# Kernel tuning notes

Hardware: AMD Instinct MI355X
Metric: run time of the kernel (lower is better)

Reference implementation:

```python
import jax, jax.numpy as jnp
import numpy as np

VEC_DIM = 64
RANK = 2


def setup_inputs() -> dict:
    key = jax.random.key(0)
    kg, km, kp = jax.random.split(key, 3)
    grid = jax.random.normal(kg, (193, 193, VEC_DIM), dtype=jnp.float32)
    # nn.init.uniform_(M.weight, -0.5, 0.5)
    M_weight = jax.random.uniform(km, (VEC_DIM, VEC_DIM), minval=-0.5, maxval=0.5, dtype=jnp.float32)
    # nn.init.uniform_(P, -0.1, 0.1)
    P = jax.random.uniform(kp, (VEC_DIM, VEC_DIM), minval=-0.1, maxval=0.1, dtype=jnp.float32)
    return {"grid": grid, "M_weight": M_weight, "P": P}


def reference(grid, M_weight, P):
    H, W, m = grid.shape
    # periods1[i,j] = periods2[i,j] = i*m + j + 2
    periods = (jnp.arange(m, dtype=jnp.float32)[:, None] * m
               + jnp.arange(m, dtype=jnp.float32)[None, :] + 2.0)  # [m, m]

    # ---- window extraction: linear mode (step=1), rank_mode='drop', rank_op='avg' ----
    nH = H - RANK + 1
    nW = W - RANK + 1
    win_sum = jax.lax.reduce_window(grid, 0.0, jax.lax.add,
                                    (RANK, RANK, 1), (1, 1, 1), 'VALID')  # [nH, nW, m]
    x_win = (win_sum / float(RANK * RANK)).reshape(nH * nW, m)  # [B, m]

    # ---- map through M (nn.Linear, no bias): y = x @ W^T ----
    x = x_win @ M_weight.T  # [B, m]

    # ---- phi_table gather: phi[k1,k2] = cos(2*pi*k1/periods) * cos(2*pi*k2/periods) ----
    two_pi = jnp.float32(2.0 * np.pi)
    k1s = jnp.arange(nH, dtype=jnp.float32)
    k2s = jnp.arange(nW, dtype=jnp.float32)
    cos1 = jnp.cos(two_pi * k1s[:, None, None] / periods)  # [nH, m, m]
    cos2 = jnp.cos(two_pi * k2s[:, None, None] / periods)  # [nW, m, m]
    phi = (cos1[:, None, :, :] * cos2[None, :, :, :]).reshape(nH * nW, m, m)  # [B, m, m]

    # ---- Nk = einsum('bj,ij,bij->bi', x, P, phi) ----
    Nk = jnp.einsum('bj,ij,bij->bi', x, P, phi)  # [B, m]
    return Nk
```

## Files before the change

### kernel.cpp

```cpp
#include <hip/hip_runtime.h>
#include <math.h>

#define NW 192
#define Wt 193
#define NMAIN 768
#define CHUNK 48

__device__ __forceinline__ float cos_revr(float num, float rcpden) {
    float rev = num * rcpden;
    rev = __builtin_amdgcn_fractf(rev);
    return __builtin_amdgcn_cosf(rev);
}

__global__ __launch_bounds__(256, 3) void k_fused(const float* __restrict__ grid,
                                                  const float* __restrict__ Mw,
                                                  const float* __restrict__ P,
                                                  float* __restrict__ out) {
    __shared__ float bufA[4096];
    __shared__ float bufB[4096];
    __shared__ float xls[CHUNK * 68];

    int bx = blockIdx.x;
    int k1  = bx >> 2;
    int k2s = (bx & 3) * CHUNK;
    int t = threadIdx.x;
    int lane = t & 63;
    int w = __builtin_amdgcn_readfirstlane(t >> 6);
    int jb = w * 16;

    #pragma unroll
    for (int r = 0; r < 4; ++r) {
        int e = r * 256 + t;
        ((float4*)bufB)[e] = ((const float4*)Mw)[e];
    }
    {
        int c = t & 63;
        const float* gb  = grid + ((size_t)k1 * Wt + k2s) * 64 + c;
        const float* gb1 = gb + (size_t)Wt * 64;
        #pragma unroll
        for (int r = 0; r < 12; ++r) {
            int p = w * 12 + r;
            float s = gb[p * 64] + gb[(p + 1) * 64]
                    + gb1[p * 64] + gb1[(p + 1) * 64];
            bufA[p * 68 + c] = 0.25f * s;
        }
    }
    __syncthreads();

    if (lane < 48) {
        int p = lane;
        float4 wv[16];
        #pragma unroll
        for (int q = 0; q < 16; ++q) wv[q] = *(const float4*)&bufA[p * 68 + 4 * q];
        #pragma unroll
        for (int r = 0; r < 16; ++r) {
            int j = jb + r;
            const float4* mrow = (const float4*)&bufB[j * 64];
            float acc = 0.f;
            #pragma unroll
            for (int q = 0; q < 16; ++q) {
                float4 mv = mrow[q];
                acc += wv[q].x * mv.x + wv[q].y * mv.y
                     + wv[q].z * mv.z + wv[q].w * mv.w;
            }
            xls[p * 68 + j] = acc;
        }
    }
    __syncthreads();

    {
        const float4* P4 = (const float4*)P;
        #pragma unroll
        for (int s = 0; s < 4; ++s) {
            int e = s * 256 + t;
            float4 v = P4[e];
            int i = e >> 4, j0 = (e & 15) * 4;
            bufA[(j0 + 0) * 64 + i] = v.x;
            bufA[(j0 + 1) * 64 + i] = v.y;
            bufA[(j0 + 2) * 64 + i] = v.z;
            bufA[(j0 + 3) * 64 + i] = v.w;
        }
    }
    __syncthreads();

    float A[16], c1v[16], ce[16], co[16];
    #pragma unroll
    for (int jl = 0; jl < 16; ++jl) {
        float T  = (float)(lane * 64 + jb + jl + 2);
        float rT = __builtin_amdgcn_rcpf(T);
        A[jl]   = 2.0f * cos_revr(1.0f, rT);
        c1v[jl] = cos_revr((float)k1, rT) * bufA[(jb + jl) * 64 + lane];
    }

    float* part = bufB;
    for (int sub = 0; sub < 3; ++sub) {
        int k2a = k2s + sub * 16;
        #pragma unroll
        for (int jl = 0; jl < 16; ++jl) {
            float T  = (float)(lane * 64 + jb + jl + 2);
            float rT = __builtin_amdgcn_rcpf(T);
            ce[jl] = cos_revr((float)k2a, rT);
            co[jl] = cos_revr((float)(k2a - 1), rT);
        }
        #pragma unroll
        for (int nn = 0; nn < 8; ++nn) {
            {
                const float4* xq = (const float4*)&xls[(sub * 16 + 2 * nn) * 68 + jb];
                float4 q0 = xq[0], q1 = xq[1], q2 = xq[2], q3 = xq[3];
                float xs[16] = {q0.x, q0.y, q0.z, q0.w, q1.x, q1.y, q1.z, q1.w,
                                q2.x, q2.y, q2.z, q2.w, q3.x, q3.y, q3.z, q3.w};
                float psum = 0.f;
                #pragma unroll
                for (int jl = 0; jl < 16; ++jl) {
                    psum   = fmaf(xs[jl] * c1v[jl], ce[jl], psum);
                    co[jl] = fmaf(A[jl], ce[jl], -co[jl]);
                }
                part[(w * 16 + 2 * nn) * 64 + lane] = psum;
            }
            {
                const float4* xq = (const float4*)&xls[(sub * 16 + 2 * nn + 1) * 68 + jb];
                float4 q0 = xq[0], q1 = xq[1], q2 = xq[2], q3 = xq[3];
                float xs[16] = {q0.x, q0.y, q0.z, q0.w, q1.x, q1.y, q1.z, q1.w,
                                q2.x, q2.y, q2.z, q2.w, q3.x, q3.y, q3.z, q3.w};
                float psum = 0.f;
                #pragma unroll
                for (int jl = 0; jl < 16; ++jl) {
                    psum   = fmaf(xs[jl] * c1v[jl], co[jl], psum);
                    ce[jl] = fmaf(A[jl], co[jl], -ce[jl]);
                }
                part[(w * 16 + 2 * nn + 1) * 64 + lane] = psum;
            }
        }
        __syncthreads();
        #pragma unroll
        for (int s = 0; s < 4; ++s) {
            int e = s * 256 + t;
            float r = part[e] + part[1024 + e] + part[2048 + e] + part[3072 + e];
            out[((size_t)k1 * NW + (k2a + (e >> 6))) * 64 + (e & 63)] = r;
        }
        __syncthreads();
    }
}

extern "C" void kernel_launch(void* const* d_in, const int* in_sizes, int n_in,
                              void* d_out, int out_size, void* d_ws, size_t ws_size,
                              hipStream_t stream) {
    const float* grid = (const float*)d_in[0];
    const float* Mw   = (const float*)d_in[1];
    const float* P    = (const float*)d_in[2];
    float* out = (float*)d_out;
    (void)d_ws; (void)ws_size;

    k_fused<<<NMAIN, 256, 0, stream>>>(grid, Mw, P, out);
}
```

Measured before the change: 95.33 us.

## Halve per-block k2 chunk, cut shared memory, raise occupancy to six blocks

Each block now handles 24 k2 positions instead of 48, which doubles the grid to 1536 blocks. Shared memory drops from two 4096-float buffers plus the x tile to one 4096 buffer plus a smaller tile, and launch bounds ask for 6 blocks per CU. The cosine recurrence is seeded once before the loop and carried across sub-chunks instead of being recomputed per sub-chunk. The x@M^T loop is restructured to accumulate in registers, and the dot product is split into two partial sums for more ILP. In exchange, the Mw, P and grid-halo loads are repeated in twice as many blocks, and the tighter register budget may cause spills.

New measurement: 246.0 us. 158% more time.

```diff
diff --git a/kernel.cpp b/kernel.cpp
--- a/kernel.cpp
+++ b/kernel.cpp
@@ -3,8 +3,9 @@
 
 #define NW 192
 #define Wt 193
-#define NMAIN 768
-#define CHUNK 48
+#define CHUNK 24
+#define NCH 8
+#define NMAIN (192*NCH)
 
 __device__ __forceinline__ float cos_revr(float num, float rcpden) {
     float rev = num * rcpden;
@@ -12,62 +13,65 @@
     return __builtin_amdgcn_cosf(rev);
 }
 
-__global__ __launch_bounds__(256, 3) void k_fused(const float* __restrict__ grid,
+__global__ __launch_bounds__(256, 6) void k_fused(const float* __restrict__ grid,
                                                   const float* __restrict__ Mw,
                                                   const float* __restrict__ P,
                                                   float* __restrict__ out) {
-    __shared__ float bufA[4096];
-    __shared__ float bufB[4096];
-    __shared__ float xls[CHUNK * 68];
+    __shared__ float buf1[4096];
+    __shared__ float buf2[CHUNK * 68];
 
     int bx = blockIdx.x;
-    int k1  = bx >> 2;
-    int k2s = (bx & 3) * CHUNK;
+    int k1  = bx >> 3;
+    int k2s = (bx & 7) * CHUNK;
     int t = threadIdx.x;
     int lane = t & 63;
     int w = __builtin_amdgcn_readfirstlane(t >> 6);
     int jb = w * 16;
 
     #pragma unroll
-    for (int r = 0; r < 4; ++r) {
-        int e = r * 256 + t;
-        ((float4*)bufB)[e] = ((const float4*)Mw)[e];
-    }
+    for (int r = 0; r < 4; ++r)
+        ((float4*)buf1)[r * 256 + t] = ((const float4*)Mw)[r * 256 + t];
     {
-        int c = t & 63;
+        int c = lane;
         const float* gb  = grid + ((size_t)k1 * Wt + k2s) * 64 + c;
         const float* gb1 = gb + (size_t)Wt * 64;
         #pragma unroll
-        for (int r = 0; r < 12; ++r) {
-            int p = w * 12 + r;
+        for (int r = 0; r < 6; ++r) {
+            int p = w * 6 + r;
             float s = gb[p * 64] + gb[(p + 1) * 64]
                     + gb1[p * 64] + gb1[(p + 1) * 64];
-            bufA[p * 68 + c] = 0.25f * s;
+            buf2[p * 68 + c] = 0.25f * s;
         }
     }
     __syncthreads();
 
-    if (lane < 48) {
-        int p = lane;
-        float4 wv[16];
+    float accj[16];
+    if (lane < CHUNK) {
         #pragma unroll
-        for (int q = 0; q < 16; ++q) wv[q] = *(const float4*)&bufA[p * 68 + 4 * q];
+        for (int r = 0; r < 16; ++r) accj[r] = 0.f;
         #pragma unroll
-        for (int r = 0; r < 16; ++r) {
-            int j = jb + r;
-            const float4* mrow = (const float4*)&bufB[j * 64];
-            float acc = 0.f;
+        for (int q4 = 0; q4 < 4; ++q4) {
+            float4 wv0 = *(const float4*)&buf2[lane * 68 + q4 * 16];
+            float4 wv1 = *(const float4*)&buf2[lane * 68 + q4 * 16 + 4];
+            float4 wv2 = *(const float4*)&buf2[lane * 68 + q4 * 16 + 8];
+            float4 wv3 = *(const float4*)&buf2[lane * 68 + q4 * 16 + 12];
             #pragma unroll
-            for (int q = 0; q < 16; ++q) {
-                float4 mv = mrow[q];
-                acc += wv[q].x * mv.x + wv[q].y * mv.y
-                     + wv[q].z * mv.z + wv[q].w * mv.w;
+            for (int r = 0; r < 16; ++r) {
+                const float4* mrow = (const float4*)&buf1[(jb + r) * 64 + q4 * 16];
+                float4 m0 = mrow[0], m1 = mrow[1], m2 = mrow[2], m3 = mrow[3];
+                accj[r] += wv0.x * m0.x + wv0.y * m0.y + wv0.z * m0.z + wv0.w * m0.w
+                         + wv1.x * m1.x + wv1.y * m1.y + wv1.z * m1.z + wv1.w * m1.w
+                         + wv2.x * m2.x + wv2.y * m2.y + wv2.z * m2.z + wv2.w * m2.w
+                         + wv3.x * m3.x + wv3.y * m3.y + wv3.z * m3.z + wv3.w * m3.w;
             }
-            xls[p * 68 + j] = acc;
         }
     }
     __syncthreads();
-
+    if (lane < CHUNK) {
+        #pragma unroll
+        for (int r = 0; r < 16; ++r)
+            buf2[lane * 68 + jb + r] = accj[r];
+    }
     {
         const float4* P4 = (const float4*)P;
         #pragma unroll
@@ -75,10 +79,10 @@
             int e = s * 256 + t;
             float4 v = P4[e];
             int i = e >> 4, j0 = (e & 15) * 4;
-            bufA[(j0 + 0) * 64 + i] = v.x;
-            bufA[(j0 + 1) * 64 + i] = v.y;
-            bufA[(j0 + 2) * 64 + i] = v.z;
-            bufA[(j0 + 3) * 64 + i] = v.w;
+            buf1[(j0 + 0) * 64 + i] = v.x;
+            buf1[(j0 + 1) * 64 + i] = v.y;
+            buf1[(j0 + 2) * 64 + i] = v.z;
+            buf1[(j0 + 3) * 64 + i] = v.w;
         }
     }
     __syncthreads();
@@ -89,54 +93,62 @@
         float T  = (float)(lane * 64 + jb + jl + 2);
         float rT = __builtin_amdgcn_rcpf(T);
         A[jl]   = 2.0f * cos_revr(1.0f, rT);
-        c1v[jl] = cos_revr((float)k1, rT) * bufA[(jb + jl) * 64 + lane];
+        c1v[jl] = cos_revr((float)k1, rT) * buf1[(jb + jl) * 64 + lane];
+        ce[jl]  = cos_revr((float)k2s, rT);
+        co[jl]  = cos_revr((float)(k2s - 1), rT);
     }
+    __syncthreads();
 
-    float* part = bufB;
-    for (int sub = 0; sub < 3; ++sub) {
-        int k2a = k2s + sub * 16;
+    float* part = buf1;
+    #pragma unroll
+    for (int sub = 0; sub < 2; ++sub) {
         #pragma unroll
-        for (int jl = 0; jl < 16; ++jl) {
-            float T  = (float)(lane * 64 + jb + jl + 2);
-            float rT = __builtin_amdgcn_rcpf(T);
-            ce[jl] = cos_revr((float)k2a, rT);
-            co[jl] = cos_revr((float)(k2a - 1), rT);
-        }
-        #pragma unroll
-        for (int nn = 0; nn < 8; ++nn) {
+        for (int m = 0; m < 6; ++m) {
             {
-                const float4* xq = (const float4*)&xls[(sub * 16 + 2 * nn) * 68 + jb];
+                int k2i = sub * 12 + 2 * m;
+                const float4* xq = (const float4*)&buf2[k2i * 68 + jb];
                 float4 q0 = xq[0], q1 = xq[1], q2 = xq[2], q3 = xq[3];
                 float xs[16] = {q0.x, q0.y, q0.z, q0.w, q1.x, q1.y, q1.z, q1.w,
                                 q2.x, q2.y, q2.z, q2.w, q3.x, q3.y, q3.z, q3.w};
-                float psum = 0.f;
+                float pa = 0.f, pb = 0.f;
                 #pragma unroll
-                for (int jl = 0; jl < 16; ++jl) {
-                    psum   = fmaf(xs[jl] * c1v[jl], ce[jl], psum);
+                for (int jl = 0; jl < 8; ++jl) {
+                    pa     = fmaf(xs[jl] * c1v[jl], ce[jl], pa);
                     co[jl] = fmaf(A[jl], ce[jl], -co[jl]);
                 }
-                part[(w * 16 + 2 * nn) * 64 + lane] = psum;
+                #pragma unroll
+                for (int jl = 8; jl < 16; ++jl) {
+                    pb     = fmaf(xs[jl] * c1v[jl], ce[jl], pb);
+                    co[jl] = fmaf(A[jl], ce[jl], -co[jl]);
+                }
+                part[(w * 12 + 2 * m) * 64 + lane] = pa + pb;
             }
             {
-                const float4* xq = (const float4*)&xls[(sub * 16 + 2 * nn + 1) * 68 + jb];
+                int k2i = sub * 12 + 2 * m + 1;
+                const float4* xq = (const float4*)&buf2[k2i * 68 + jb];
                 float4 q0 = xq[0], q1 = xq[1], q2 = xq[2], q3 = xq[3];
                 float xs[16] = {q0.x, q0.y, q0.z, q0.w, q1.x, q1.y, q1.z, q1.w,
                                 q2.x, q2.y, q2.z, q2.w, q3.x, q3.y, q3.z, q3.w};
-                float psum = 0.f;
+                float pa = 0.f, pb = 0.f;
                 #pragma unroll
-                for (int jl = 0; jl < 16; ++jl) {
-                    psum   = fmaf(xs[jl] * c1v[jl], co[jl], psum);
+                for (int jl = 0; jl < 8; ++jl) {
+                    pa     = fmaf(xs[jl] * c1v[jl], co[jl], pa);
                     ce[jl] = fmaf(A[jl], co[jl], -ce[jl]);
                 }
-                part[(w * 16 + 2 * nn + 1) * 64 + lane] = psum;
+                #pragma unroll
+                for (int jl = 8; jl < 16; ++jl) {
+                    pb     = fmaf(xs[jl] * c1v[jl], co[jl], pb);
+                    ce[jl] = fmaf(A[jl], co[jl], -ce[jl]);
+                }
+                part[(w * 12 + 2 * m + 1) * 64 + lane] = pa + pb;
             }
         }
         __syncthreads();
         #pragma unroll
-        for (int s = 0; s < 4; ++s) {
+        for (int s = 0; s < 3; ++s) {
             int e = s * 256 + t;
-            float r = part[e] + part[1024 + e] + part[2048 + e] + part[3072 + e];
-            out[((size_t)k1 * NW + (k2a + (e >> 6))) * 64 + (e & 63)] = r;
+            float r = part[e] + part[768 + e] + part[1536 + e] + part[2304 + e];
+            out[((size_t)k1 * NW + (k2s + sub * 12 + (e >> 6))) * 64 + (e & 63)] = r;
         }
         __syncthreads();
     }
```
